# Kernel tuning notes

Hardware: AMD Instinct MI355X
Metric: run time of the kernel (lower is better)

Reference implementation:

```python
import jax, jax.numpy as jnp
import numpy as np

T, N, D_OBS = 32, 32, 64
HID, HEADS, MEM, N_ACT = 512, 4, 128, 16
SECTIONS = [HEADS * HID, HEADS, HID, 1, HID, HID, HEADS, 1, 1, 3 * HEADS]
XI = sum(SECTIONS)


def setup_inputs() -> dict:
    key = jax.random.key(0)
    ks = jax.random.split(key, 8)
    s = 0.02
    return {
        "inputs": jax.random.normal(ks[0], (T, N, D_OBS), jnp.float32),
        "w_ih": jax.random.normal(ks[1], (3 * HID, D_OBS), jnp.float32) * s,
        "w_hh": jax.random.normal(ks[2], (3 * HID, HID), jnp.float32) * s,
        "b_ih": jnp.zeros((3 * HID,), jnp.float32),
        "b_hh": jnp.zeros((3 * HID,), jnp.float32),
        "Wf": jax.random.normal(ks[3], (XI, HID), jnp.float32) * s,
        "bf": jnp.zeros((XI,), jnp.float32),
        "Wa": jax.random.normal(ks[4], (N_ACT, HID), jnp.float32) * s,
        "ba": jnp.zeros((N_ACT,), jnp.float32),
        "Wc": jax.random.normal(ks[5], (1, HID), jnp.float32) * s,
        "bc": jnp.zeros((1,), jnp.float32),
    }


def reference(inputs, w_ih, w_hh, b_ih, b_hh, Wf, bf, Wa, ba, Wc, bc):
    idx = np.cumsum(SECTIONS)[:-1]
    eps = 1e-8

    def step(carry, x_t):
        h, wr, u, ww, M, p, L = carry
        # --- GRU cell (torch convention) ---
        gi = x_t @ w_ih.T + b_ih
        gh = h @ w_hh.T + b_hh
        ir, iz, inn = jnp.split(gi, 3, axis=-1)
        hr, hz, hn = jnp.split(gh, 3, axis=-1)
        rg = jax.nn.sigmoid(ir + hr)
        zg = jax.nn.sigmoid(iz + hz)
        ng = jnp.tanh(inn + rg * hn)
        h = (1 - zg) * ng + zg * h
        # --- interface vector xi ---
        xi = jax.nn.relu(h) @ Wf.T + bf
        Kr, Br, kw, bw, e, v, F_hat, ga, gw, Pi = jnp.split(xi, idx, axis=-1)
        Kr = Kr.reshape(N, HEADS, HID)
        Br = jax.nn.softplus(Br)                      # [N,H]
        bw = jax.nn.softplus(bw)                      # [N,1]
        e = jax.nn.sigmoid(e)                         # [N,HID] erase
        v_w = v                                       # [N,HID] write vec
        F_hat = jax.nn.sigmoid(F_hat)                 # [N,H] free gates
        ga = jax.nn.sigmoid(ga)                       # [N,1]
        gw = jax.nn.sigmoid(gw)                       # [N,1]
        Pi = jax.nn.softmax(Pi.reshape(N, HEADS, 3), axis=-1)
        # --- memory retention & usage ---
        psi = jnp.prod(1 - F_hat[..., None] * wr, axis=1)          # [N,MEM]
        u = (u + ww - u * ww) * psi
        # --- allocation weighting via usage sort ---
        phi = jnp.argsort(u, axis=-1)
        u_sorted = jnp.take_along_axis(u, phi, axis=-1)
        excl = jnp.concatenate(
            [jnp.ones((N, 1), u.dtype), jnp.cumprod(u_sorted[:, :-1], axis=-1)], axis=-1)
        a_sorted = (1 - u_sorted) * excl
        alloc = jnp.zeros_like(u).at[jnp.arange(N)[:, None], phi].set(a_sorted)
        # --- content-based write weighting ---
        Mn = jnp.sqrt(jnp.sum(M * M, axis=-1))                     # [N,MEM]
        kwn = jnp.sqrt(jnp.sum(kw * kw, axis=-1, keepdims=True))   # [N,1]
        cos_w = jnp.einsum('nmd,nd->nm', M, kw) / (Mn * kwn + eps)
        cw = jax.nn.softmax(bw * cos_w, axis=-1)
        ww = gw * (ga * alloc + (1 - ga) * cw)                     # [N,MEM]
        # --- memory write (erase + add outer products) ---
        M = M * (1 - ww[..., None] * e[:, None, :]) + ww[..., None] * v_w[:, None, :]
        # --- precedence & temporal link matrix ---
        p = (1 - jnp.sum(ww, axis=-1, keepdims=True)) * p + ww
        L = (1 - ww[..., None] - ww[:, None, :]) * L + ww[..., None] * p[:, None, :]
        # --- forward/backward read weights ---
        fwd_w = jnp.einsum('nij,nhj->nhi', L, wr)
        bwd_w = jnp.einsum('nji,nhj->nhi', L, wr)
        # --- content-based read weighting ---
        Mn2 = jnp.sqrt(jnp.sum(M * M, axis=-1))                    # [N,MEM]
        Krn = jnp.sqrt(jnp.sum(Kr * Kr, axis=-1, keepdims=True))   # [N,H,1]
        cos_r = jnp.einsum('nmd,nhd->nhm', M, Kr) / (Mn2[:, None, :] * Krn + eps)
        cr = jax.nn.softmax(Br[..., None] * cos_r, axis=-1)
        wr = Pi[..., 0:1] * bwd_w + Pi[..., 1:2] * cr + Pi[..., 2:3] * fwd_w
        # --- read vectors, actor, critic ---
        r_read = jnp.einsum('nmd,nhm->nd', M, wr)                  # sum over heads -> [N,HID]
        a_probs = jax.nn.softmax(r_read @ Wa.T + ba, axis=-1)      # [N,N_ACT]
        val = h @ Wc.T + bc                                        # [N,1]
        return (h, wr, u, ww, M, p, L), jnp.concatenate([a_probs, val], axis=-1)

    z = jnp.zeros
    carry0 = (z((N, HID)), z((N, HEADS, MEM)), z((N, MEM)), z((N, MEM)),
              z((N, MEM, HID)), z((N, MEM)), z((N, MEM, MEM)))
    _, outs = jax.lax.scan(step, carry0, inputs)
    return outs  # [T, N, N_ACT+1]
```

## Files before the change

### kernel.cpp

```cpp
#include <hip/hip_runtime.h>
#include <math.h>

#define TT 32
#define NB 32
#define DOBS 64
#define HID 512
#define HEADS 4
#define MEM 128
#define NACT 16
#define XID 3607
#define G3 1536

__device__ __forceinline__ float sigm(float x){ return 1.0f/(1.0f+__expf(-x)); }
__device__ __forceinline__ float splus(float x){ return fmaxf(x,0.f) + log1pf(__expf(-fabsf(x))); }

__device__ __forceinline__ float wsum64(float s){
    s += __shfl_xor(s,1); s += __shfl_xor(s,2); s += __shfl_xor(s,4);
    s += __shfl_xor(s,8); s += __shfl_xor(s,16);
    float t = s;
    asm volatile("v_permlane32_swap_b32 %0, %1" : "+v"(s), "+v"(t));
    return s + t;
}
__device__ __forceinline__ float rsum_hi(float v){
    float t = v;
    asm volatile("v_permlane16_swap_b32 %0, %1" : "+v"(v), "+v"(t));
    v += t;
    float t2 = v;
    asm volatile("v_permlane32_swap_b32 %0, %1" : "+v"(v), "+v"(t2));
    return v + t2;
}

__global__ __launch_bounds__(256) void k_transpose(const float* __restrict__ src,
                                                   float* __restrict__ dst, int R, int C)
{
    __shared__ float tile[32][33];
    int r0 = blockIdx.x*32, c0 = blockIdx.y*32;
    int tx = threadIdx.x, ty = threadIdx.y;
    #pragma unroll
    for (int yy = 0; yy < 32; yy += 8) {
        int r = r0 + ty + yy, c = c0 + tx;
        if (r < R && c < C) tile[ty+yy][tx] = src[(size_t)r*C + c];
    }
    __syncthreads();
    #pragma unroll
    for (int yy = 0; yy < 32; yy += 8) {
        int c = c0 + ty + yy, r = r0 + tx;
        if (r < R && c < C) dst[(size_t)c*R + r] = tile[tx][ty+yy];
    }
}

__global__ __launch_bounds__(384) void k_gru(
    const float* __restrict__ x,
    const float* __restrict__ wihT,
    const float* __restrict__ whhT,
    const float* __restrict__ b_ih,
    const float* __restrict__ b_hh,
    float* __restrict__ h_all,
    float* hG,
    int* flags)
{
    const int n   = blockIdx.x & 31;
    const int s   = blockIdx.x >> 5;
    const int tid = threadIdx.x;
    const int kq  = tid / 96;
    const int c   = tid % 96;
    const int g   = c >> 5;
    const int r0  = g*512 + s*128 + (c & 31)*4;

    __shared__ float hS[512];
    __shared__ float xS[64];
    __shared__ float4 pI[4][96];
    __shared__ float4 pH[4][96];
    __shared__ float grS[128], gzS[128], giN[128], ghN[128];

    for (int i = tid; i < 512; i += 384) hS[i] = 0.f;

    for (int t = 0; t < TT; ++t) {
        if (tid < 64) xS[tid] = x[((size_t)t*NB + n)*DOBS + tid];
        __syncthreads();
        {
            float4 aI = make_float4(0.f,0.f,0.f,0.f);
            float4 aH = make_float4(0.f,0.f,0.f,0.f);
            const int kx0 = kq*16;
            #pragma unroll 4
            for (int k = kx0; k < kx0+16; ++k) {
                float xv = xS[k];
                float4 w = *(const float4*)(wihT + (size_t)k*G3 + r0);
                aI.x += w.x*xv; aI.y += w.y*xv; aI.z += w.z*xv; aI.w += w.w*xv;
            }
            const int kh0 = kq*128;
            #pragma unroll 4
            for (int k = kh0; k < kh0+128; ++k) {
                float hv = hS[k];
                float4 w = *(const float4*)(whhT + (size_t)k*G3 + r0);
                aH.x += w.x*hv; aH.y += w.y*hv; aH.z += w.z*hv; aH.w += w.w*hv;
            }
            pI[kq][c] = aI; pH[kq][c] = aH;
        }
        __syncthreads();
        {
            const int g2 = tid >> 7, d = tid & 127;
            const int c2 = g2*32 + (d>>2), e = d & 3;
            float AI = 0.f, AH = 0.f;
            #pragma unroll
            for (int q = 0; q < 4; ++q) {
                float4 vi = pI[q][c2], vh = pH[q][c2];
                AI += (e==0)?vi.x:(e==1)?vi.y:(e==2)?vi.z:vi.w;
                AH += (e==0)?vh.x:(e==1)?vh.y:(e==2)?vh.z:vh.w;
            }
            const int rg = g2*512 + s*128 + d;
            AI += b_ih[rg]; AH += b_hh[rg];
            if (g2 == 0)      grS[d] = AI + AH;
            else if (g2 == 1) gzS[d] = AI + AH;
            else              { giN[d] = AI; ghN[d] = AH; }
        }
        __syncthreads();
        if (tid < 128) {
            const int D = s*128 + tid;
            float rg = sigm(grS[tid]);
            float zg = sigm(gzS[tid]);
            float ng = tanhf(giN[tid] + rg*ghN[tid]);
            float hn = (1.f-zg)*ng + zg*hS[D];
            h_all[((size_t)t*NB + n)*HID + D] = hn;
            __hip_atomic_store(&hG[n*HID + D], hn, __ATOMIC_RELAXED, __HIP_MEMORY_SCOPE_AGENT);
        }
        __syncthreads();
        if (t+1 < TT) {
            if (tid == 0) {
                __hip_atomic_fetch_add(&flags[n], 1, __ATOMIC_RELEASE, __HIP_MEMORY_SCOPE_AGENT);
                while (__hip_atomic_load(&flags[n], __ATOMIC_ACQUIRE, __HIP_MEMORY_SCOPE_AGENT) < 4*(t+1)) {
                    __builtin_amdgcn_s_sleep(4);
                }
            }
            __syncthreads();
            for (int i = tid; i < 512; i += 384)
                hS[i] = __hip_atomic_load(&hG[n*HID + i], __ATOMIC_RELAXED, __HIP_MEMORY_SCOPE_AGENT);
        }
    }
}

__global__ __launch_bounds__(256) void k_xi(
    const float* __restrict__ h_all,
    const float* __restrict__ Wf,
    const float* __restrict__ bf,
    float* __restrict__ xi_all)
{
    __shared__ float As[16][132];
    __shared__ float Bs[16][68];
    const int jt = blockIdx.x * 64;
    const int it = blockIdx.y * 128;
    const int tid = threadIdx.x;
    const int lc = tid & 15, lr = tid >> 4;
    const int tx = tid & 15, ty = tid >> 4;
    float acc[8][4] = {};

    for (int k0 = 0; k0 < HID; k0 += 16) {
        #pragma unroll
        for (int s = 0; s < 8; ++s) {
            int i = lr*8 + s;
            As[lc][i] = fmaxf(h_all[(size_t)(it + i)*HID + k0 + lc], 0.f);
        }
        #pragma unroll
        for (int s = 0; s < 4; ++s) {
            int j = lr*4 + s;
            Bs[lc][j] = (jt + j < XID) ? Wf[(size_t)(jt + j)*HID + k0 + lc] : 0.f;
        }
        __syncthreads();
        #pragma unroll
        for (int k = 0; k < 16; ++k) {
            float a[8], b[4];
            #pragma unroll
            for (int u = 0; u < 8; ++u) a[u] = As[k][ty*8+u];
            #pragma unroll
            for (int v = 0; v < 4; ++v) b[v] = Bs[k][tx*4+v];
            #pragma unroll
            for (int u = 0; u < 8; ++u)
                #pragma unroll
                for (int v = 0; v < 4; ++v) acc[u][v] += a[u]*b[v];
        }
        __syncthreads();
    }
    #pragma unroll
    for (int u = 0; u < 8; ++u)
        #pragma unroll
        for (int v = 0; v < 4; ++v) {
            int i = it + ty*8 + u, j = jt + tx*4 + v;
            if (j < XID) xi_all[(size_t)i*XID + j] = acc[u][v] + bf[j];
        }
}

__global__ __launch_bounds__(64) void k_val(
    const float* __restrict__ h_all, const float* __restrict__ Wc,
    const float* __restrict__ bc, float* __restrict__ out)
{
    const int row = blockIdx.x;
    const int lane = threadIdx.x;
    float acc = 0.f;
    for (int d = lane; d < HID; d += 64) acc += h_all[(size_t)row*HID + d]*Wc[d];
    for (int off = 32; off; off >>= 1) acc += __shfl_down(acc, off);
    if (lane == 0) out[(size_t)row*17 + 16] = acc + bc[0];
}

#define LPAD 132
#define SROW2 576
#define DYN_FLOATS (128*LPAD + 16*SROW2)
#define CIDX(d) ((((d)>>6)*68) + ((d)&63))
#define CIDX2(d) ((((d)>>5)*36) + ((d)&31))

__global__ __launch_bounds__(1024) void k_mem(
    const float* __restrict__ xi_all,
    const float* __restrict__ Wa,
    const float* __restrict__ ba,
    float* __restrict__ out)
{
    extern __shared__ __align__(16) float dynS[];
    float* Lm  = dynS;
    float* scr = dynS + 128*LPAD;

    const int n = blockIdx.x;
    const int tid = threadIdx.x;
    const int lane = tid & 63;
    const int wv = tid >> 6;
    const int m8 = tid >> 3;
    const int q8 = tid & 7;
    const int rp = tid >> 4;
    const int ch = tid & 15;
    const int r0 = rp*2, r1 = r0+1;

    __shared__ __align__(16) float KrC[4*576];
    __shared__ __align__(16) float kwC[576], eC[576], vC[576];
    __shared__ __align__(16) float wrC[4*136];
    __shared__ __align__(16) float r_S[512];
    __shared__ float dotK_S[4][132], fwd_S[4][132], bwd_S[4][132];
    __shared__ float u_S[128], ww_S[128], p_S[128], cw_S[128], srt_S[128], aS_S[128];
    __shared__ float Mn2_S[128], dw_S[128];
    __shared__ int   rk_S[128];
    __shared__ float wred[16][6];
    __shared__ float scal_S[8];
    __shared__ float PiRaw[12];
    __shared__ float Pi_S[4][3], Br_S[4], KrN_S[4], F_S[4];
    __shared__ float ba_S[16], logit_S[16];

    float4 Mreg[16];
    #pragma unroll
    for (int i = 0; i < 16; ++i) Mreg[i] = make_float4(0.f,0.f,0.f,0.f);

    for (int i = tid; i < 128*LPAD; i += 1024) Lm[i] = 0.f;
    if (tid < 16) ba_S[tid] = ba[tid];
    if (tid < 128) { u_S[tid]=0.f; ww_S[tid]=0.f; p_S[tid]=0.f; Mn2_S[tid]=0.f; }
    if (tid < 512) wrC[(tid>>7)*136 + CIDX(tid&127)] = 0.f;

    float waR[8];
    #pragma unroll
    for (int j = 0; j < 8; ++j) waR[j] = Wa[(wv<<9) + lane + (j<<6)];

    const bool hasEx = (tid >= 1000 && tid < 1023);
    int exIdx = 0;
    if (tid >= 1000 && tid < 1004)      exIdx = 2048 + (tid - 1000);
    else if (tid == 1004)               exIdx = 2564;
    else if (tid >= 1005 && tid < 1023) exIdx = 3589 + (tid - 1005);

    const float* xi0 = xi_all + (size_t)n*XID;
    float pKrA = xi0[tid];
    float pKrB = xi0[1024 + tid];
    float pkw = 0.f, pv = 0.f, pe = 0.f;
    if (tid < 512) { pkw = xi0[2052 + tid]; pv = xi0[3077 + tid]; }
    else           { pe  = xi0[2565 + (tid - 512)]; }
    float pex = hasEx ? xi0[exIdx] : 0.f;
    __syncthreads();

    for (int t = 0; t < TT; ++t) {
        float ev2 = 0.f;

        {
            int d = tid & 511, hh = tid >> 9;
            int co = CIDX2(d);
            KrC[hh*576 + co]     = pKrA;
            KrC[(2+hh)*576 + co] = pKrB;
        }
        if (tid < 512) { int co = CIDX2(tid); kwC[co] = pkw; vC[co] = pv; }
        else { int s2 = tid - 512; eC[CIDX2(s2)] = sigm(pe); }
        if (hasEx) {
            if (tid < 1004)      Br_S[tid-1000] = splus(pex);
            else if (tid==1004)  scal_S[0] = splus(pex);
            else if (tid < 1009) F_S[tid-1005] = sigm(pex);
            else if (tid==1009)  scal_S[1] = sigm(pex);
            else if (tid==1010)  scal_S[2] = sigm(pex);
            else                 PiRaw[tid-1011] = pex;
        }
        {
            float sA = wsum64(pKrA*pKrA);
            float sB = wsum64(pKrB*pKrB);
            float sK = wsum64(pkw*pkw);
            if (lane == 0) { wred[wv][0]=sA; wred[wv][1]=sB; wred[wv][2]=sK; }
        }
        {
            int tn = (t+1 < TT) ? (t+1) : t;
            const float* xin = xi_all + (size_t)(tn*NB + n)*XID;
            pKrA = xin[tid]; pKrB = xin[1024 + tid];
            if (tid < 512) { pkw = xin[2052 + tid]; pv = xin[3077 + tid]; }
            else           { pe  = xin[2565 + (tid - 512)]; }
            if (hasEx) pex = xin[exIdx];
        }
        __syncthreads();

        if (tid < 4) {
            float s = 0.f;
            #pragma unroll
            for (int w = 0; w < 8; ++w) s += wred[(tid&1)*8 + w][tid>>1];
            KrN_S[tid] = sqrtf(s);
        } else if (tid == 4) {
            float s = 0.f;
            #pragma unroll
            for (int w = 0; w < 8; ++w) s += wred[w][2];
            scal_S[3] = sqrtf(s);
        }
        if (tid < 128) {
            int co = CIDX(tid);
            float psi = (1.f - F_S[0]*wrC[co])      * (1.f - F_S[1]*wrC[136+co])
                      * (1.f - F_S[2]*wrC[272+co])  * (1.f - F_S[3]*wrC[408+co]);
            float uu = u_S[tid], w = ww_S[tid];
            u_S[tid] = (uu + w - uu*w)*psi;
        }
        {
            const float* kwp = kwC + ch*36;
            float dw0 = 0.f, dw1 = 0.f;
            #pragma unroll
            for (int c = 0; c < 8; ++c) {
                float4 kk = *(const float4*)(kwp + 4*c);
                float4 x0 = Mreg[c], x1 = Mreg[8+c];
                dw0 += x0.x*kk.x + x0.y*kk.y + x0.z*kk.z + x0.w*kk.w;
                dw1 += x1.x*kk.x + x1.y*kk.y + x1.z*kk.z + x1.w*kk.w;
            }
            dw0 += __shfl_xor(dw0,1); dw0 += __shfl_xor(dw0,2); dw0 += __shfl_xor(dw0,4); dw0 += __shfl_xor(dw0,8);
            dw1 += __shfl_xor(dw1,1); dw1 += __shfl_xor(dw1,2); dw1 += __shfl_xor(dw1,4); dw1 += __shfl_xor(dw1,8);
            if (ch == 0) { dw_S[r0] = dw0; dw_S[r1] = dw1; }
        }
        __syncthreads();

        {
            float um = u_S[m8];
            int rk = 0;
            #pragma unroll
            for (int jj = 0; jj < 16; ++jj) {
                int j = jj*8 + q8;
                float uj = u_S[j];
                rk += (uj < um || (uj == um && j < m8)) ? 1 : 0;
            }
            rk += __shfl_xor(rk,1); rk += __shfl_xor(rk,2); rk += __shfl_xor(rk,4);
            if (q8 == 0) { rk_S[m8] = rk; srt_S[rk] = um; }
        }
        if (tid < 128) {
            float cwv = scal_S[0]*dw_S[tid]/(Mn2_S[tid]*scal_S[3] + 1e-8f);
            float ev = __expf(cwv);
            cw_S[tid] = ev;
            float s = wsum64(ev);
            if (lane == 0) wred[wv][1] = s;
        } else if (tid >= 136 && tid < 140) {
            int h = tid - 136;
            float p0 = PiRaw[3*h], p1 = PiRaw[3*h+1], p2 = PiRaw[3*h+2];
            float mx = fmaxf(p0, fmaxf(p1, p2));
            float e0=__expf(p0-mx), e1=__expf(p1-mx), e2=__expf(p2-mx);
            float s = e0+e1+e2;
            Pi_S[h][0]=e0/s; Pi_S[h][1]=e1/s; Pi_S[h][2]=e2/s;
        }
        __syncthreads();

        if (wv == 0) {
            float x0 = srt_S[2*lane], x1 = srt_S[2*lane+1];
            float pp = x0*x1;
            float sc = pp;
            #pragma unroll
            for (int off = 1; off < 64; off <<= 1) {
                float y = __shfl_up(sc, off);
                if (lane >= off) sc *= y;
            }
            float excl = __shfl_up(sc, 1);
            if (lane == 0) excl = 1.f;
            aS_S[2*lane]   = (1.f - x0)*excl;
            aS_S[2*lane+1] = (1.f - x1)*excl*x0;
        }
        __syncthreads();

        if (tid < 128) {
            float cwsum = wred[0][1] + wred[1][1];
            float alloc = aS_S[rk_S[tid]];
            float ga = scal_S[1], gw = scal_S[2];
            float w = gw*(ga*alloc + (1.f-ga)*cw_S[tid]/cwsum);
            ww_S[tid] = w;
            float s = wsum64(w);
            if (lane == 0) wred[wv][0] = s;
        }
        __syncthreads();

        if (tid < 128) {
            float sww = wred[0][0] + wred[1][0];
            p_S[tid] = (1.f - sww)*p_S[tid] + ww_S[tid];
        }
        {
            const int base = ch*36;
            const float* ep  = eC + base;
            const float* vp  = vC + base;
            const float* k0p = KrC + base;
            const float* k1p = KrC + 576 + base;
            const float* k2p = KrC + 1152 + base;
            const float* k3p = KrC + 1728 + base;
            const float ww0 = ww_S[r0], ww1 = ww_S[r1];
            float nrm0=0.f, nrm1=0.f;
            float a0=0.f,a1=0.f,a2=0.f,a3=0.f;
            float b0=0.f,b1=0.f,b2=0.f,b3=0.f;
            #pragma unroll
            for (int c = 0; c < 8; ++c) {
                float4 ee = *(const float4*)(ep + 4*c);
                float4 vv = *(const float4*)(vp + 4*c);
                float4 x  = Mreg[c];
                x.x = x.x*(1.f - ww0*ee.x) + ww0*vv.x;
                x.y = x.y*(1.f - ww0*ee.y) + ww0*vv.y;
                x.z = x.z*(1.f - ww0*ee.z) + ww0*vv.z;
                x.w = x.w*(1.f - ww0*ee.w) + ww0*vv.w;
                Mreg[c] = x;
                nrm0 += x.x*x.x + x.y*x.y + x.z*x.z + x.w*x.w;
                float4 y  = Mreg[8+c];
                y.x = y.x*(1.f - ww1*ee.x) + ww1*vv.x;
                y.y = y.y*(1.f - ww1*ee.y) + ww1*vv.y;
                y.z = y.z*(1.f - ww1*ee.z) + ww1*vv.z;
                y.w = y.w*(1.f - ww1*ee.w) + ww1*vv.w;
                Mreg[8+c] = y;
                nrm1 += y.x*y.x + y.y*y.y + y.z*y.z + y.w*y.w;
                float4 k0 = *(const float4*)(k0p + 4*c);
                float4 k1 = *(const float4*)(k1p + 4*c);
                float4 k2 = *(const float4*)(k2p + 4*c);
                float4 k3 = *(const float4*)(k3p + 4*c);
                a0 += x.x*k0.x + x.y*k0.y + x.z*k0.z + x.w*k0.w;
                a1 += x.x*k1.x + x.y*k1.y + x.z*k1.z + x.w*k1.w;
                a2 += x.x*k2.x + x.y*k2.y + x.z*k2.z + x.w*k2.w;
                a3 += x.x*k3.x + x.y*k3.y + x.z*k3.z + x.w*k3.w;
                b0 += y.x*k0.x + y.y*k0.y + y.z*k0.z + y.w*k0.w;
                b1 += y.x*k1.x + y.y*k1.y + y.z*k1.z + y.w*k1.w;
                b2 += y.x*k2.x + y.y*k2.y + y.z*k2.z + y.w*k2.w;
                b3 += y.x*k3.x + y.y*k3.y + y.z*k3.z + y.w*k3.w;
            }
            #pragma unroll
            for (int mk = 1; mk < 16; mk <<= 1) {
                nrm0 += __shfl_xor(nrm0,mk); nrm1 += __shfl_xor(nrm1,mk);
                a0 += __shfl_xor(a0,mk); a1 += __shfl_xor(a1,mk);
                a2 += __shfl_xor(a2,mk); a3 += __shfl_xor(a3,mk);
                b0 += __shfl_xor(b0,mk); b1 += __shfl_xor(b1,mk);
                b2 += __shfl_xor(b2,mk); b3 += __shfl_xor(b3,mk);
            }
            if (ch < 4) {
                float dA = (ch==0)?a0:(ch==1)?a1:(ch==2)?a2:a3;
                float dB = (ch==0)?b0:(ch==1)?b1:(ch==2)?b2:b3;
                dotK_S[ch][r0] = dA;
                dotK_S[ch][r1] = dB;
            } else if (ch == 4) {
                Mn2_S[r0] = sqrtf(nrm0);
                Mn2_S[r1] = sqrtf(nrm1);
            }
        }
        __syncthreads();

        {
            const int j2 = tid & 127, w8 = tid >> 7;
            float wwj = ww_S[j2], pj = p_S[j2];
            float b0=0.f,b1=0.f,b2=0.f,b3=0.f;
            #pragma unroll
            for (int c2 = 0; c2 < 4; ++c2) {
                const int rr0 = (w8<<4) + (c2<<2);
                const int bidx = CIDX(rr0);
                float4 wwv = *(const float4*)&ww_S[rr0];
                float4 w0v = *(const float4*)&wrC[bidx];
                float4 w1v = *(const float4*)&wrC[136+bidx];
                float4 w2v = *(const float4*)&wrC[272+bidx];
                float4 w3v = *(const float4*)&wrC[408+bidx];
                #pragma unroll
                for (int s4 = 0; s4 < 4; ++s4) {
                    int i2 = rr0 + s4;
                    float wwi = (s4==0)?wwv.x:(s4==1)?wwv.y:(s4==2)?wwv.z:wwv.w;
                    float lold = Lm[i2*LPAD + j2];
                    float ln = (1.f - wwi - wwj)*lold + wwi*pj;
                    Lm[i2*LPAD + j2] = ln;
                    b0 += ln*((s4==0)?w0v.x:(s4==1)?w0v.y:(s4==2)?w0v.z:w0v.w);
                    b1 += ln*((s4==0)?w1v.x:(s4==1)?w1v.y:(s4==2)?w1v.z:w1v.w);
                    b2 += ln*((s4==0)?w2v.x:(s4==1)?w2v.y:(s4==2)?w2v.z:w2v.w);
                    b3 += ln*((s4==0)?w3v.x:(s4==1)?w3v.y:(s4==2)?w3v.z:w3v.w);
                }
            }
            float* sp = scr + w8*SROW2 + j2;
            sp[0]=b0; sp[132]=b1; sp[264]=b2; sp[396]=b3;
        }
        __syncthreads();

        if (tid < 512) {
            int h = tid>>7, mm = tid&127;
            float s = 0.f;
            #pragma unroll
            for (int g = 0; g < 8; ++g) s += scr[g*SROW2 + h*132 + mm];
            bwd_S[h][mm] = s;
        }
        {
            const float* Lr = Lm + m8*LPAD + q8*16;
            const int wb = ((q8>>2)*68) + ((q8&3)<<4);
            float f0=0.f,f1=0.f,f2=0.f,f3=0.f;
            #pragma unroll
            for (int c = 0; c < 4; ++c) {
                float4 lv = *(const float4*)(Lr + 4*c);
                float4 w0 = *(const float4*)&wrC[wb + 4*c];
                float4 w1 = *(const float4*)&wrC[136 + wb + 4*c];
                float4 w2 = *(const float4*)&wrC[272 + wb + 4*c];
                float4 w3 = *(const float4*)&wrC[408 + wb + 4*c];
                f0 += lv.x*w0.x + lv.y*w0.y + lv.z*w0.z + lv.w*w0.w;
                f1 += lv.x*w1.x + lv.y*w1.y + lv.z*w1.z + lv.w*w1.w;
                f2 += lv.x*w2.x + lv.y*w2.y + lv.z*w2.z + lv.w*w2.w;
                f3 += lv.x*w3.x + lv.y*w3.y + lv.z*w3.z + lv.w*w3.w;
            }
            f0 += __shfl_xor(f0,1); f0 += __shfl_xor(f0,2); f0 += __shfl_xor(f0,4);
            f1 += __shfl_xor(f1,1); f1 += __shfl_xor(f1,2); f1 += __shfl_xor(f1,4);
            f2 += __shfl_xor(f2,1); f2 += __shfl_xor(f2,2); f2 += __shfl_xor(f2,4);
            f3 += __shfl_xor(f3,1); f3 += __shfl_xor(f3,2); f3 += __shfl_xor(f3,4);
            if (q8 < 4) fwd_S[q8][m8] = (q8==0) ? f0 : ((q8==1) ? f1 : ((q8==2) ? f2 : f3));
        }
        if (tid < 512) {
            int h = tid>>7, mm = tid&127;
            float scv = Br_S[h]*dotK_S[h][mm]/(Mn2_S[mm]*KrN_S[h] + 1e-8f);
            ev2 = __expf(scv);
            float s = wsum64(ev2);
            if (lane == 0) wred[wv][1] = s;
        }
        __syncthreads();

        if (tid < 512) {
            int h = tid>>7, mm = tid&127;
            float hsum = wred[2*h][1] + wred[2*h+1][1];
            float cr = ev2/hsum;
            wrC[h*136 + CIDX(mm)] = Pi_S[h][0]*bwd_S[h][mm] + Pi_S[h][1]*cr + Pi_S[h][2]*fwd_S[h][mm];
        }
        __syncthreads();

        {
            const int co0 = CIDX(r0), co1 = CIDX(r1);
            float s0 = wrC[co0] + wrC[136+co0] + wrC[272+co0] + wrC[408+co0];
            float s1 = wrC[co1] + wrC[136+co1] + wrC[272+co1] + wrC[408+co1];
            float* sp = scr + wv*SROW2 + ch*36;
            #pragma unroll
            for (int c = 0; c < 8; ++c) {
                float4 x = Mreg[c], y = Mreg[8+c];
                float px = rsum_hi(s0*x.x + s1*y.x);
                float py = rsum_hi(s0*x.y + s1*y.y);
                float pz = rsum_hi(s0*x.z + s1*y.z);
                float pw = rsum_hi(s0*x.w + s1*y.w);
                if (lane < 16) *(float4*)(sp + 4*c) = make_float4(px,py,pz,pw);
            }
        }
        __syncthreads();

        if (tid < 512) {
            int off = CIDX2(tid);
            float r = 0.f;
            #pragma unroll
            for (int w = 0; w < 16; ++w) r += scr[w*SROW2 + off];
            r_S[tid] = r;
        }
        __syncthreads();

        {
            float acc = 0.f;
            #pragma unroll
            for (int j = 0; j < 8; ++j) acc += waR[j]*r_S[lane + (j<<6)];
            acc = wsum64(acc);
            if (lane == 0) logit_S[wv] = acc + ba_S[wv];
        }
        __syncthreads();

        if (tid < 16) {
            float lg = logit_S[tid];
            float mx = lg;
            mx = fmaxf(mx, __shfl_xor(mx,1)); mx = fmaxf(mx, __shfl_xor(mx,2));
            mx = fmaxf(mx, __shfl_xor(mx,4)); mx = fmaxf(mx, __shfl_xor(mx,8));
            float ex2 = __expf(lg - mx);
            float s = ex2;
            s += __shfl_xor(s,1); s += __shfl_xor(s,2);
            s += __shfl_xor(s,4); s += __shfl_xor(s,8);
            out[(size_t)(t*NB + n)*17 + tid] = ex2/s;
        }
    }
}

extern "C" void kernel_launch(void* const* d_in, const int* in_sizes, int n_in,
                              void* d_out, int out_size, void* d_ws, size_t ws_size,
                              hipStream_t stream) {
    const float* inp  = (const float*)d_in[0];
    const float* w_ih = (const float*)d_in[1];
    const float* w_hh = (const float*)d_in[2];
    const float* b_ih = (const float*)d_in[3];
    const float* b_hh = (const float*)d_in[4];
    const float* Wf   = (const float*)d_in[5];
    const float* bf   = (const float*)d_in[6];
    const float* Wa   = (const float*)d_in[7];
    const float* ba   = (const float*)d_in[8];
    const float* Wc   = (const float*)d_in[9];
    const float* bc   = (const float*)d_in[10];
    float* out = (float*)d_out;

    float* ws = (float*)d_ws;
    float* wihT   = ws;
    float* whhT   = ws + 98304;
    float* h_all  = ws + 884736;
    float* xi_all = ws + 1409024;
    float* hG     = ws + 5102592;
    int*   flags  = (int*)(ws + 5119008);

    static int dynset = 0;
    if (!dynset) {
        hipFuncSetAttribute(reinterpret_cast<const void*>(k_mem),
                            hipFuncAttributeMaxDynamicSharedMemorySize,
                            DYN_FLOATS*4);
        dynset = 1;
    }

    hipMemsetAsync(flags, 0, NB*sizeof(int), stream);

    dim3 tb(32, 8);
    k_transpose<<<dim3(48, 2),  tb, 0, stream>>>(w_ih, wihT, G3, DOBS);
    k_transpose<<<dim3(48, 16), tb, 0, stream>>>(w_hh, whhT, G3, HID);
    k_gru<<<NB*4, 384, 0, stream>>>(inp, wihT, whhT, b_ih, b_hh, h_all, hG, flags);
    k_xi<<<dim3(57, 8), 256, 0, stream>>>(h_all, Wf, bf, xi_all);
    k_val<<<TT*NB, 64, 0, stream>>>(h_all, Wc, bc, out);
    k_mem<<<NB, 1024, DYN_FLOATS*4, stream>>>(xi_all, Wa, ba, out);
}
```

Measured before the change: 1.273 ms.

## Split GRU across 8 blocks per batch, compute allocation without sort

```diff
diff --git a/kernel.cpp b/kernel.cpp
--- a/kernel.cpp
+++ b/kernel.cpp
@@ -62,16 +62,16 @@
     const int n   = blockIdx.x & 31;
     const int s   = blockIdx.x >> 5;
     const int tid = threadIdx.x;
-    const int kq  = tid / 96;
-    const int c   = tid % 96;
-    const int g   = c >> 5;
-    const int r0  = g*512 + s*128 + (c & 31)*4;
+    const int kq  = tid / 48;
+    const int c   = tid % 48;
+    const int g   = c >> 4;
+    const int r0  = g*512 + s*64 + (c & 15)*4;
 
     __shared__ float hS[512];
     __shared__ float xS[64];
-    __shared__ float4 pI[4][96];
-    __shared__ float4 pH[4][96];
-    __shared__ float grS[128], gzS[128], giN[128], ghN[128];
+    __shared__ float4 pI[8][48];
+    __shared__ float4 pH[8][48];
+    __shared__ float grS[64], gzS[64], giN[64], ghN[64];
 
     for (int i = tid; i < 512; i += 384) hS[i] = 0.f;
 
@@ -81,16 +81,16 @@
         {
             float4 aI = make_float4(0.f,0.f,0.f,0.f);
             float4 aH = make_float4(0.f,0.f,0.f,0.f);
-            const int kx0 = kq*16;
+            const int kx0 = kq*8;
             #pragma unroll 4
-            for (int k = kx0; k < kx0+16; ++k) {
+            for (int k = kx0; k < kx0+8; ++k) {
                 float xv = xS[k];
                 float4 w = *(const float4*)(wihT + (size_t)k*G3 + r0);
                 aI.x += w.x*xv; aI.y += w.y*xv; aI.z += w.z*xv; aI.w += w.w*xv;
             }
-            const int kh0 = kq*128;
+            const int kh0 = kq*64;
             #pragma unroll 4
-            for (int k = kh0; k < kh0+128; ++k) {
+            for (int k = kh0; k < kh0+64; ++k) {
                 float hv = hS[k];
                 float4 w = *(const float4*)(whhT + (size_t)k*G3 + r0);
                 aH.x += w.x*hv; aH.y += w.y*hv; aH.z += w.z*hv; aH.w += w.w*hv;
@@ -98,25 +98,25 @@
             pI[kq][c] = aI; pH[kq][c] = aH;
         }
         __syncthreads();
-        {
-            const int g2 = tid >> 7, d = tid & 127;
-            const int c2 = g2*32 + (d>>2), e = d & 3;
+        if (tid < 192) {
+            const int g2 = tid >> 6, d = tid & 63;
+            const int c2 = g2*16 + (d>>2), e = d & 3;
             float AI = 0.f, AH = 0.f;
             #pragma unroll
-            for (int q = 0; q < 4; ++q) {
+            for (int q = 0; q < 8; ++q) {
                 float4 vi = pI[q][c2], vh = pH[q][c2];
                 AI += (e==0)?vi.x:(e==1)?vi.y:(e==2)?vi.z:vi.w;
                 AH += (e==0)?vh.x:(e==1)?vh.y:(e==2)?vh.z:vh.w;
             }
-            const int rg = g2*512 + s*128 + d;
+            const int rg = g2*512 + s*64 + d;
             AI += b_ih[rg]; AH += b_hh[rg];
             if (g2 == 0)      grS[d] = AI + AH;
             else if (g2 == 1) gzS[d] = AI + AH;
             else              { giN[d] = AI; ghN[d] = AH; }
         }
         __syncthreads();
-        if (tid < 128) {
-            const int D = s*128 + tid;
+        if (tid < 64) {
+            const int D = s*64 + tid;
             float rg = sigm(grS[tid]);
             float zg = sigm(gzS[tid]);
             float ng = tanhf(giN[tid] + rg*ghN[tid]);
@@ -128,7 +128,7 @@
         if (t+1 < TT) {
             if (tid == 0) {
                 __hip_atomic_fetch_add(&flags[n], 1, __ATOMIC_RELEASE, __HIP_MEMORY_SCOPE_AGENT);
-                while (__hip_atomic_load(&flags[n], __ATOMIC_ACQUIRE, __HIP_MEMORY_SCOPE_AGENT) < 4*(t+1)) {
+                while (__hip_atomic_load(&flags[n], __ATOMIC_ACQUIRE, __HIP_MEMORY_SCOPE_AGENT) < 8*(t+1)) {
                     __builtin_amdgcn_s_sleep(4);
                 }
             }
@@ -232,9 +232,8 @@
     __shared__ __align__(16) float wrC[4*136];
     __shared__ __align__(16) float r_S[512];
     __shared__ float dotK_S[4][132], fwd_S[4][132], bwd_S[4][132];
-    __shared__ float u_S[128], ww_S[128], p_S[128], cw_S[128], srt_S[128], aS_S[128];
+    __shared__ float u_S[128], ww_S[128], p_S[128], aS_S[128];
     __shared__ float Mn2_S[128], dw_S[128];
-    __shared__ int   rk_S[128];
     __shared__ float wred[16][6];
     __shared__ float scal_S[8];
     __shared__ float PiRaw[12];
@@ -270,7 +269,7 @@
     __syncthreads();
 
     for (int t = 0; t < TT; ++t) {
-        float ev2 = 0.f;
+        float ev2 = 0.f, evA = 0.f;
 
         {
             int d = tid & 511, hh = tid >> 9;
@@ -340,21 +339,22 @@
 
         {
             float um = u_S[m8];
-            int rk = 0;
+            float pr = 1.f;
             #pragma unroll
             for (int jj = 0; jj < 16; ++jj) {
                 int j = jj*8 + q8;
                 float uj = u_S[j];
-                rk += (uj < um || (uj == um && j < m8)) ? 1 : 0;
-            }
-            rk += __shfl_xor(rk,1); rk += __shfl_xor(rk,2); rk += __shfl_xor(rk,4);
-            if (q8 == 0) { rk_S[m8] = rk; srt_S[rk] = um; }
+                pr *= ((uj < um) || (uj == um && j < m8)) ? uj : 1.f;
+            }
+            pr *= __shfl_xor(pr, 1);
+            pr *= __shfl_xor(pr, 2);
+            pr *= __shfl_xor(pr, 4);
+            if (q8 == 0) aS_S[m8] = (1.f - um)*pr;
         }
         if (tid < 128) {
             float cwv = scal_S[0]*dw_S[tid]/(Mn2_S[tid]*scal_S[3] + 1e-8f);
-            float ev = __expf(cwv);
-            cw_S[tid] = ev;
-            float s = wsum64(ev);
+            evA = __expf(cwv);
+            float s = wsum64(evA);
             if (lane == 0) wred[wv][1] = s;
         } else if (tid >= 136 && tid < 140) {
             int h = tid - 136;
@@ -366,27 +366,11 @@
         }
         __syncthreads();
 
-        if (wv == 0) {
-            float x0 = srt_S[2*lane], x1 = srt_S[2*lane+1];
-            float pp = x0*x1;
-            float sc = pp;
-            #pragma unroll
-            for (int off = 1; off < 64; off <<= 1) {
-                float y = __shfl_up(sc, off);
-                if (lane >= off) sc *= y;
-            }
-            float excl = __shfl_up(sc, 1);
-            if (lane == 0) excl = 1.f;
-            aS_S[2*lane]   = (1.f - x0)*excl;
-            aS_S[2*lane+1] = (1.f - x1)*excl*x0;
-        }
-        __syncthreads();
-
         if (tid < 128) {
             float cwsum = wred[0][1] + wred[1][1];
-            float alloc = aS_S[rk_S[tid]];
+            float alloc = aS_S[tid];
             float ga = scal_S[1], gw = scal_S[2];
-            float w = gw*(ga*alloc + (1.f-ga)*cw_S[tid]/cwsum);
+            float w = gw*(ga*alloc + (1.f-ga)*evA/cwsum);
             ww_S[tid] = w;
             float s = wsum64(w);
             if (lane == 0) wred[wv][0] = s;
@@ -554,12 +538,15 @@
         }
         __syncthreads();
 
-        if (tid < 512) {
-            int off = CIDX2(tid);
-            float r = 0.f;
-            #pragma unroll
-            for (int w = 0; w < 16; ++w) r += scr[w*SROW2 + off];
-            r_S[tid] = r;
+        if (tid < 128) {
+            const int off = CIDX2(tid<<2);
+            float4 r = make_float4(0.f,0.f,0.f,0.f);
+            #pragma unroll
+            for (int w = 0; w < 16; ++w) {
+                float4 v = *(const float4*)&scr[w*SROW2 + off];
+                r.x += v.x; r.y += v.y; r.z += v.z; r.w += v.w;
+            }
+            *(float4*)&r_S[tid<<2] = r;
         }
         __syncthreads();
 
@@ -623,7 +610,7 @@
     dim3 tb(32, 8);
     k_transpose<<<dim3(48, 2),  tb, 0, stream>>>(w_ih, wihT, G3, DOBS);
     k_transpose<<<dim3(48, 16), tb, 0, stream>>>(w_hh, whhT, G3, HID);
-    k_gru<<<NB*4, 384, 0, stream>>>(inp, wihT, whhT, b_ih, b_hh, h_all, hG, flags);
+    k_gru<<<NB*8, 384, 0, stream>>>(inp, wihT, whhT, b_ih, b_hh, h_all, hG, flags);
     k_xi<<<dim3(57, 8), 256, 0, stream>>>(h_all, Wf, bf, xi_all);
     k_val<<<TT*NB, 64, 0, stream>>>(h_all, Wc, bc, out);
     k_mem<<<NB, 1024, DYN_FLOATS*4, stream>>>(xi_all, Wa, ba, out);
```

Result: faster. 1.244 ms (-2.3%).
